# Optimization experiments

Hardware: AMD Instinct MI355X
Metric: run time of the kernel (lower is better)

Reference implementation:

```python
import jax, jax.numpy as jnp
import numpy as np

D = 1024   # hidden
H = 4      # heads
HD = D // H
E = 8      # experts
FF = 4096  # expert ffn dim
CAP_FACTOR = 1.0


def _ln(x, g, b, eps=1e-5):
    mu = jnp.mean(x, -1, keepdims=True)
    v = jnp.mean((x - mu) ** 2, -1, keepdims=True)
    return (x - mu) * jax.lax.rsqrt(v + eps) * g + b


def setup_inputs() -> dict:
    key = jax.random.key(0)
    ks = jax.random.split(key, 8)
    L, N = 1024, 16
    s = 0.02
    return {
        "x": jax.random.normal(ks[0], (L, N, D), jnp.float32),
        "in_proj_w": jax.random.normal(ks[1], (3 * D, D), jnp.float32) * s,
        "in_proj_b": jnp.zeros((3 * D,), jnp.float32),
        "out_proj_w": jax.random.normal(ks[2], (D, D), jnp.float32) * s,
        "out_proj_b": jnp.zeros((D,), jnp.float32),
        "ln1_g": jnp.ones((D,), jnp.float32),
        "ln1_b": jnp.zeros((D,), jnp.float32),
        "ln2_g": jnp.ones((D,), jnp.float32),
        "ln2_b": jnp.zeros((D,), jnp.float32),
        "wg": jax.random.normal(ks[3], (D, E), jnp.float32) * s,
        "w1": jax.random.normal(ks[4], (E, D, FF), jnp.float32) * s,
        "b1": jnp.zeros((E, FF), jnp.float32),
        "w2": jax.random.normal(ks[5], (E, FF, D), jnp.float32) * s,
        "b2": jnp.zeros((E, D), jnp.float32),
    }


def _mha(x, w, b, ow, ob):
    # x: [L, N, D] (torch MultiheadAttention layout, batch_first=False)
    L, N, _ = x.shape
    qkv = x @ w.T + b
    q, k, v = jnp.split(qkv, 3, axis=-1)
    rh = lambda t: t.reshape(L, N, H, HD).transpose(1, 2, 0, 3)  # -> [N,H,L,HD]
    q, k, v = rh(q), rh(k), rh(v)
    scores = jnp.einsum('nhld,nhmd->nhlm', q, k) / np.float32(np.sqrt(HD))
    attn = jax.nn.softmax(scores, axis=-1)
    o = jnp.einsum('nhlm,nhmd->nhld', attn, v).transpose(2, 0, 1, 3).reshape(L, N, D)
    return o @ ow.T + ob


def _moe(x, wg, w1, b1, w2, b2):
    # top-1 switch gating with capacity drop, dispatch, grouped GEMM, combine
    L, N, _ = x.shape
    S = L * N
    cap = int(CAP_FACTOR * S) // E  # 2048
    xf = x.reshape(S, D)
    gates = jax.nn.softmax(xf @ wg, axis=-1)           # [S,E]
    idx = jnp.argmax(gates, axis=-1)                    # [S] top-1 expert
    mask1 = jax.nn.one_hot(idx, E, dtype=x.dtype)       # [S,E]
    # position of each token within its expert's queue
    loc = jnp.sum((jnp.cumsum(mask1, 0) - 1.0) * mask1, -1).astype(jnp.int32)
    keep = loc < cap                                    # capacity drop mask
    gate_val = jnp.take_along_axis(gates, idx[:, None], -1)[:, 0]
    slot = jnp.where(keep, idx.astype(jnp.int32) * cap + loc, E * cap)  # OOB if dropped
    disp = jnp.zeros((E * cap, D), x.dtype).at[slot].set(xf, mode='drop')
    disp = disp.reshape(E, cap, D)
    # expert = Linear(D,FF) -> Linear(FF,D), NO activation between (per source)
    h = jnp.einsum('ecd,edf->ecf', disp, w1) + b1[:, None, :]
    y = (jnp.einsum('ecf,efd->ecd', h, w2) + b2[:, None, :]).reshape(E * cap, D)
    out = jnp.where(keep[:, None], gate_val[:, None] * y[jnp.minimum(slot, E * cap - 1)], 0.0)
    return out.reshape(L, N, D)


def reference(x, in_proj_w, in_proj_b, out_proj_w, out_proj_b,
              ln1_g, ln1_b, ln2_g, ln2_b, wg, w1, b1, w2, b2):
    y1 = _ln(x + _mha(x, in_proj_w, in_proj_b, out_proj_w, out_proj_b), ln1_g, ln1_b)
    y2 = _ln(y1 + _moe(y1, wg, w1, b1, w2, b2), ln2_g, ln2_b)
    return y2
```

## Files before the change

### kernel.cpp

```cpp
#include <hip/hip_runtime.h>
#include <hip/hip_bf16.h>

typedef __bf16 bf16_t;
typedef bf16_t bf16x4 __attribute__((ext_vector_type(4)));
typedef bf16_t bf16x8 __attribute__((ext_vector_type(8)));
typedef float  f32x4  __attribute__((ext_vector_type(4)));
typedef _Float16 half4 __attribute__((ext_vector_type(4)));
typedef _Float16 half8 __attribute__((ext_vector_type(8)));

#define L_  1024
#define N_  16
#define S_  16384
#define D_  1024
#define H_  4
#define HD_ 256
#define E_  8
#define FF_ 4096
#define CAP_ 2048
#define ESLOTS_ (E_*CAP_)
#define TAU_ 0.03f

__device__ __forceinline__ void gload16(const void* g, void* l) {
  __builtin_amdgcn_global_load_lds(
      (const __attribute__((address_space(1))) void*)g,
      (__attribute__((address_space(3))) void*)l,
      16, 0, 0);
}

#define SRC_SWZ(lane) (((lane) & 3) ^ (((lane) >> 3) & 3))

__global__ __launch_bounds__(256) void split2(
    const float* __restrict__ in, _Float16* __restrict__ oh,
    _Float16* __restrict__ ol, long n4)
{
  long i = (long)blockIdx.x * blockDim.x + threadIdx.x;
  long stride = (long)gridDim.x * blockDim.x;
  for (; i < n4; i += stride) {
    float4 v = ((const float4*)in)[i];
    half4 h, l;
    h.x = (_Float16)v.x; l.x = (_Float16)((v.x - (float)h.x) * 4096.0f);
    h.y = (_Float16)v.y; l.y = (_Float16)((v.y - (float)h.y) * 4096.0f);
    h.z = (_Float16)v.z; l.z = (_Float16)((v.z - (float)h.z) * 4096.0f);
    h.w = (_Float16)v.w; l.w = (_Float16)((v.w - (float)h.w) * 4096.0f);
    ((half4*)oh)[i] = h;
    ((half4*)ol)[i] = l;
  }
}

template<int EPI, bool HAS_BIAS, int PROD>
__global__ __launch_bounds__(256) void hgemm3s(
    const _Float16* __restrict__ Ah, const _Float16* __restrict__ Al,
    const _Float16* __restrict__ Bh, const _Float16* __restrict__ Bl,
    float* __restrict__ Cf, _Float16* __restrict__ Ch, _Float16* __restrict__ Cl,
    const float* __restrict__ bias,
    int K, long lda, long ldb, long ldcf, long ldch,
    int Z2, long sA1, long sA2, long sB1, long sB2, long sC1, long sC2, long sBias)
{
  constexpr int NL   = (PROD == 3) ? 2 : 1;
  constexpr int NBUF = (PROD == 3) ? 2 : 3;
  __shared__ _Float16 tA[NL][NBUF][128 * 32];
  __shared__ _Float16 tB[NL][NBUF][64 * 32];
  const int z  = blockIdx.z;
  const int z1 = z / Z2, z2 = z - z1 * Z2;
  const long aoff = (long)z1 * sA1 + (long)z2 * sA2;
  const long boff = (long)z1 * sB1 + (long)z2 * sB2;
  const long coff = (long)z1 * sC1 + (long)z2 * sC2;
  const int brow = blockIdx.y * 128, bcol = blockIdx.x * 64;
  const int tid = threadIdx.x, lane = tid & 63, wid = tid >> 6;
  const int wr = (wid >> 1) * 64, wc = (wid & 1) * 32;
  const int fr = lane & 15;
  const int fqs = (((lane >> 4) ^ ((fr >> 1) & 3)) * 8);

  const bool isA = (wid < 2);
  int limb, dstoff, nch;
  const _Float16* ssrc;
  if constexpr (PROD == 3) {
    limb = wid & 1; nch = isA ? 8 : 4; dstoff = 0;
    ssrc = (wid == 0) ? Ah : (wid == 1) ? Al : (wid == 2) ? Bh : Bl;
  } else {
    limb = 0; nch = isA ? 4 : 2; dstoff = (wid & 1) * nch;
    ssrc = isA ? Ah : Bh;
  }
  const long sld = isA ? lda : ldb;
  const long soff = isA ? aoff : boff;
  int srow = (isA ? brow : bcol) + (lane >> 2);
  if constexpr (PROD == 1) srow += (wid & 1) * (isA ? 64 : 32);
  const _Float16* sbase = ssrc + soff + (long)srow * sld + SRC_SWZ(lane) * 8;

  f32x4 acc0[4][2], acc1[4][2];
#pragma unroll
  for (int mi = 0; mi < 4; ++mi)
#pragma unroll
    for (int ni = 0; ni < 2; ++ni) {
      acc0[mi][ni] = f32x4{0.f, 0.f, 0.f, 0.f};
      acc1[mi][ni] = f32x4{0.f, 0.f, 0.f, 0.f};
    }

  const int NT = K >> 5;

  if constexpr (PROD == 3) {
    {
      _Float16* d0 = (isA ? &tA[limb][0][0] : &tB[limb][0][0]) + dstoff * 512;
      for (int i = 0; i < nch; ++i)
        gload16(sbase + (long)(16 * i) * sld, d0 + i * 512);
    }
    __syncthreads();

    for (int t = 0; t < NT; ++t) {
      const int cur = t & 1;
      if (t + 1 < NT) {
        const int k1 = (t + 1) * 32;
        _Float16* d0 = (isA ? &tA[limb][cur ^ 1][0] : &tB[limb][cur ^ 1][0]) + dstoff * 512;
        for (int i = 0; i < nch; ++i)
          gload16(sbase + (long)(16 * i) * sld + k1, d0 + i * 512);
      }

      half8 bh_[2], bl_[2];
#pragma unroll
      for (int ni = 0; ni < 2; ++ni) {
        bh_[ni] = *(const half8*)&tB[0][cur][(wc + ni * 16 + fr) * 32 + fqs];
        bl_[ni] = *(const half8*)&tB[1][cur][(wc + ni * 16 + fr) * 32 + fqs];
      }
      half8 ah_[4], al_[4];
#pragma unroll
      for (int mi = 0; mi < 4; ++mi) {
        ah_[mi] = *(const half8*)&tA[0][cur][(wr + mi * 16 + fr) * 32 + fqs];
        al_[mi] = *(const half8*)&tA[1][cur][(wr + mi * 16 + fr) * 32 + fqs];
      }
#pragma unroll
      for (int mi = 0; mi < 4; ++mi)
#pragma unroll
        for (int ni = 0; ni < 2; ++ni)
          acc0[mi][ni] = __builtin_amdgcn_mfma_f32_16x16x32_f16(ah_[mi], bh_[ni], acc0[mi][ni], 0, 0, 0);
#pragma unroll
      for (int mi = 0; mi < 4; ++mi)
#pragma unroll
        for (int ni = 0; ni < 2; ++ni)
          acc1[mi][ni] = __builtin_amdgcn_mfma_f32_16x16x32_f16(ah_[mi], bl_[ni], acc1[mi][ni], 0, 0, 0);
#pragma unroll
      for (int mi = 0; mi < 4; ++mi)
#pragma unroll
        for (int ni = 0; ni < 2; ++ni)
          acc1[mi][ni] = __builtin_amdgcn_mfma_f32_16x16x32_f16(al_[mi], bh_[ni], acc1[mi][ni], 0, 0, 0);
      __syncthreads();
    }
  } else {
    {
      _Float16* d0 = (isA ? &tA[0][0][0] : &tB[0][0][0]) + dstoff * 512;
      for (int i = 0; i < nch; ++i)
        gload16(sbase + (long)(16 * i) * sld, d0 + i * 512);
      _Float16* d1 = (isA ? &tA[0][1][0] : &tB[0][1][0]) + dstoff * 512;
      for (int i = 0; i < nch; ++i)
        gload16(sbase + (long)(16 * i) * sld + 32, d1 + i * 512);
    }
    if (isA) asm volatile("s_waitcnt vmcnt(4)" ::: "memory");
    else     asm volatile("s_waitcnt vmcnt(2)" ::: "memory");
    __builtin_amdgcn_s_barrier();

    for (int t = 0; t < NT; ++t) {
      const int b = t % 3;
      if (t + 2 < NT) {
        const int k2 = (t + 2) * 32;
        const int b2 = (t + 2) % 3;
        _Float16* d0 = (isA ? &tA[0][b2][0] : &tB[0][b2][0]) + dstoff * 512;
        for (int i = 0; i < nch; ++i)
          gload16(sbase + (long)(16 * i) * sld + k2, d0 + i * 512);
      }

      half8 bh_[2];
#pragma unroll
      for (int ni = 0; ni < 2; ++ni)
        bh_[ni] = *(const half8*)&tB[0][b][(wc + ni * 16 + fr) * 32 + fqs];
      half8 ah_[4];
#pragma unroll
      for (int mi = 0; mi < 4; ++mi)
        ah_[mi] = *(const half8*)&tA[0][b][(wr + mi * 16 + fr) * 32 + fqs];
#pragma unroll
      for (int mi = 0; mi < 4; ++mi)
#pragma unroll
        for (int ni = 0; ni < 2; ++ni)
          acc0[mi][ni] = __builtin_amdgcn_mfma_f32_16x16x32_f16(ah_[mi], bh_[ni], acc0[mi][ni], 0, 0, 0);

      if (t + 1 < NT) {
        if (t + 2 < NT) {
          if (isA) asm volatile("s_waitcnt vmcnt(4)" ::: "memory");
          else     asm volatile("s_waitcnt vmcnt(2)" ::: "memory");
        } else {
          asm volatile("s_waitcnt vmcnt(0)" ::: "memory");
        }
        __builtin_amdgcn_s_barrier();
      }
    }
  }

#pragma unroll
  for (int mi = 0; mi < 4; ++mi) {
#pragma unroll
    for (int ni = 0; ni < 2; ++ni) {
      int gcol = bcol + wc + ni * 16 + fr;
      float bv = 0.0f;
      if constexpr (HAS_BIAS) bv = bias[(long)z1 * sBias + gcol];
#pragma unroll
      for (int v = 0; v < 4; ++v) {
        int grow = brow + wr + mi * 16 + (lane >> 4) * 4 + v;
        float val = acc0[mi][ni][v] + bv;
        if constexpr (PROD == 3) val += acc1[mi][ni][v] * 0.000244140625f;
        if constexpr (EPI == 0) {
          Cf[coff + (long)grow * ldcf + gcol] = val;
        } else if constexpr (EPI == 1) {
          _Float16 hh = (_Float16)val;
          _Float16 ll = (_Float16)((val - (float)hh) * 4096.0f);
          long ci = coff + (long)grow * ldch + gcol;
          Ch[ci] = hh; Cl[ci] = ll;
        } else if constexpr (EPI == 3) {
          Ch[coff + (long)grow * ldch + gcol] = (_Float16)val;
        } else {
          if (bcol < 2048) {
            _Float16 hh = (_Float16)val;
            _Float16 ll = (_Float16)((val - (float)hh) * 4096.0f);
            long ci = (long)grow * ldch + gcol;
            Ch[ci] = hh; Cl[ci] = ll;
          } else {
            Cf[(long)grow * ldcf + (gcol - 2048)] = val;
          }
        }
      }
    }
  }
}

template<bool OUT_BF16, bool HAS_BIAS>
__global__ __launch_bounds__(256) void bgemm16(
    const bf16_t* __restrict__ A, const bf16_t* __restrict__ B,
    void* __restrict__ Cout, const float* __restrict__ bias,
    int K, long lda, long ldb, long ldc,
    long sA1, long sB1, long sC1, long sBias)
{
  __shared__ bf16_t tiles[2][3][128 * 32];
  const int z = blockIdx.z;
  const long coff = (long)z * sC1;
  const int brow = blockIdx.y * 128, bcol = blockIdx.x * 128;
  const int tid = threadIdx.x, lane = tid & 63, wid = tid >> 6;
  const int wr = (wid >> 1) * 64, wc = (wid & 1) * 64;
  const int fr = lane & 15;
  const int fqs = (((lane >> 4) ^ ((fr >> 1) & 3)) * 8);

  const bf16_t* src0 = (wid < 2) ? (A + (long)z * sA1) : (B + (long)z * sB1);
  const long ld = (wid < 2) ? lda : ldb;
  const int  rb = ((wid < 2) ? brow : bcol) + 64 * (wid & 1) + (lane >> 2);
  const bf16_t* srcbase = src0 + (long)rb * ld + SRC_SWZ(lane) * 8;
  const int tsel = wid >> 1, halfsel = wid & 1;

  f32x4 acc[4][4];
#pragma unroll
  for (int mi = 0; mi < 4; ++mi)
#pragma unroll
    for (int ni = 0; ni < 4; ++ni)
      acc[mi][ni] = f32x4{0.0f, 0.0f, 0.0f, 0.0f};

  const int NT = K >> 5;

#pragma unroll
  for (int i = 0; i < 4; ++i)
    gload16(srcbase + (long)(16 * i) * ld, &tiles[tsel][0][(4 * halfsel + i) * 512]);
#pragma unroll
  for (int i = 0; i < 4; ++i)
    gload16(srcbase + (long)(16 * i) * ld + 32, &tiles[tsel][1][(4 * halfsel + i) * 512]);
  asm volatile("s_waitcnt vmcnt(4)" ::: "memory");
  __builtin_amdgcn_s_barrier();

  for (int t = 0; t < NT; ++t) {
    const int b = t % 3;
    if (t + 2 < NT) {
      const int k2 = (t + 2) * 32;
      const int b2 = (t + 2) % 3;
#pragma unroll
      for (int i = 0; i < 4; ++i)
        gload16(srcbase + (long)(16 * i) * ld + k2, &tiles[tsel][b2][(4 * halfsel + i) * 512]);
    }

    bf16x8 af[4], bfv[4];
#pragma unroll
    for (int i = 0; i < 4; ++i) {
      af[i]  = *(const bf16x8*)&tiles[0][b][(wr + i * 16 + fr) * 32 + fqs];
      bfv[i] = *(const bf16x8*)&tiles[1][b][(wc + i * 16 + fr) * 32 + fqs];
    }
#pragma unroll
    for (int mi = 0; mi < 4; ++mi)
#pragma unroll
      for (int ni = 0; ni < 4; ++ni)
        acc[mi][ni] = __builtin_amdgcn_mfma_f32_16x16x32_bf16(af[mi], bfv[ni], acc[mi][ni], 0, 0, 0);

    if (t + 1 < NT) {
      if (t + 2 < NT) asm volatile("s_waitcnt vmcnt(4)" ::: "memory");
      else            asm volatile("s_waitcnt vmcnt(0)" ::: "memory");
      __builtin_amdgcn_s_barrier();
    }
  }

#pragma unroll
  for (int mi = 0; mi < 4; ++mi) {
#pragma unroll
    for (int ni = 0; ni < 4; ++ni) {
      int gcol = bcol + wc + ni * 16 + fr;
      float bv = 0.0f;
      if constexpr (HAS_BIAS) bv = bias[(long)z * sBias + gcol];
#pragma unroll
      for (int v = 0; v < 4; ++v) {
        int grow = brow + wr + mi * 16 + (lane >> 4) * 4 + v;
        float val = acc[mi][ni][v] + bv;
        long ci = coff + (long)grow * ldc + gcol;
        if constexpr (OUT_BF16) ((bf16_t*)Cout)[ci] = (bf16_t)val;
        else                    ((float*)Cout)[ci]  = val;
      }
    }
  }
}

template<typename TOUT>
__global__ __launch_bounds__(256) void transpose_f32(
    const float* __restrict__ src, TOUT* __restrict__ dst,
    long ld_src, long ld_dst, int Z2,
    long ss1, long ss2, long sd1, long sd2)
{
  __shared__ float t[32][33];
  const int z = blockIdx.z, z1 = z / Z2, z2 = z - z1 * Z2;
  src += (long)z1 * ss1 + (long)z2 * ss2;
  dst += (long)z1 * sd1 + (long)z2 * sd2;
  const int c0 = blockIdx.x * 32, r0 = blockIdx.y * 32;
  const int tx = threadIdx.x & 31, ty = threadIdx.x >> 5;
#pragma unroll
  for (int i = 0; i < 4; ++i)
    t[ty + i * 8][tx] = src[(long)(r0 + ty + i * 8) * ld_src + c0 + tx];
  __syncthreads();
#pragma unroll
  for (int i = 0; i < 4; ++i)
    dst[(long)(c0 + ty + i * 8) * ld_dst + r0 + tx] = (TOUT)t[tx][ty + i * 8];
}

__global__ __launch_bounds__(256) void transpose_split(
    const float* __restrict__ src, _Float16* __restrict__ dh, _Float16* __restrict__ dl,
    long ld_src, long ld_dst, int Z2,
    long ss1, long ss2, long sd1, long sd2)
{
  __shared__ float t[32][33];
  const int z = blockIdx.z, z1 = z / Z2, z2 = z - z1 * Z2;
  src += (long)z1 * ss1 + (long)z2 * ss2;
  dh  += (long)z1 * sd1 + (long)z2 * sd2;
  dl  += (long)z1 * sd1 + (long)z2 * sd2;
  const int c0 = blockIdx.x * 32, r0 = blockIdx.y * 32;
  const int tx = threadIdx.x & 31, ty = threadIdx.x >> 5;
#pragma unroll
  for (int i = 0; i < 4; ++i)
    t[ty + i * 8][tx] = src[(long)(r0 + ty + i * 8) * ld_src + c0 + tx];
  __syncthreads();
#pragma unroll
  for (int i = 0; i < 4; ++i) {
    float v = t[tx][ty + i * 8];
    _Float16 h = (_Float16)v;
    _Float16 l = (_Float16)((v - (float)h) * 4096.0f);
    long idx = (long)(c0 + ty + i * 8) * ld_dst + r0 + tx;
    dh[idx] = h;
    dl[idx] = l;
  }
}

__global__ __launch_bounds__(256) void softmax16(
    _Float16* __restrict__ Sm, float scale)
{
  __shared__ float red[4];
  const long row = blockIdx.x;
  half4* p = (half4*)(Sm + row * 1024);
  const int tid = threadIdx.x;
  half4 hv = p[tid];
  float v0 = (float)hv.x, v1 = (float)hv.y, v2 = (float)hv.z, v3 = (float)hv.w;
  float m = fmaxf(fmaxf(v0, v1), fmaxf(v2, v3));
#pragma unroll
  for (int o = 32; o; o >>= 1) m = fmaxf(m, __shfl_xor(m, o, 64));
  if ((tid & 63) == 0) red[tid >> 6] = m;
  __syncthreads();
  m = fmaxf(fmaxf(red[0], red[1]), fmaxf(red[2], red[3]));
  __syncthreads();
  float e0 = __expf((v0 - m) * scale);
  float e1 = __expf((v1 - m) * scale);
  float e2 = __expf((v2 - m) * scale);
  float e3 = __expf((v3 - m) * scale);
  float s = e0 + e1 + e2 + e3;
#pragma unroll
  for (int o = 32; o; o >>= 1) s += __shfl_xor(s, o, 64);
  if ((tid & 63) == 0) red[tid >> 6] = s;
  __syncthreads();
  s = red[0] + red[1] + red[2] + red[3];
  float inv = 1.0f / s;
  half4 w;
  w.x = (_Float16)(e0 * inv); w.y = (_Float16)(e1 * inv);
  w.z = (_Float16)(e2 * inv); w.w = (_Float16)(e3 * inv);
  p[tid] = w;
}

template<bool WRITE_LO>
__global__ __launch_bounds__(256) void softmax_pack(
    float* __restrict__ Sm, float scale)
{
  __shared__ float red[4];
  const long row = blockIdx.x;
  const float4* p = (const float4*)(Sm + row * 1024);
  const int tid = threadIdx.x;
  float4 v = p[tid];
  float m = fmaxf(fmaxf(v.x, v.y), fmaxf(v.z, v.w));
#pragma unroll
  for (int o = 32; o; o >>= 1) m = fmaxf(m, __shfl_xor(m, o, 64));
  if ((tid & 63) == 0) red[tid >> 6] = m;
  __syncthreads();
  m = fmaxf(fmaxf(red[0], red[1]), fmaxf(red[2], red[3]));
  __syncthreads();
  float e0 = __expf((v.x - m) * scale);
  float e1 = __expf((v.y - m) * scale);
  float e2 = __expf((v.z - m) * scale);
  float e3 = __expf((v.w - m) * scale);
  float s = e0 + e1 + e2 + e3;
#pragma unroll
  for (int o = 32; o; o >>= 1) s += __shfl_xor(s, o, 64);
  if ((tid & 63) == 0) red[tid >> 6] = s;
  __syncthreads();
  s = red[0] + red[1] + red[2] + red[3];
  float inv = 1.0f / s;
  float p0 = e0 * inv, p1 = e1 * inv, p2 = e2 * inv, p3 = e3 * inv;
  half4 h;
  h.x = (_Float16)p0; h.y = (_Float16)p1; h.z = (_Float16)p2; h.w = (_Float16)p3;
  _Float16* base = (_Float16*)Sm + row * 2048;
  ((half4*)base)[tid] = h;
  if constexpr (WRITE_LO) {
    half4 l;
    l.x = (_Float16)((p0 - (float)h.x) * 4096.0f);
    l.y = (_Float16)((p1 - (float)h.y) * 4096.0f);
    l.z = (_Float16)((p2 - (float)h.z) * 4096.0f);
    l.w = (_Float16)((p3 - (float)h.w) * 4096.0f);
    ((half4*)(base + 1024))[tid] = l;
  }
}

__global__ __launch_bounds__(256) void add_ln_gate(
    const float* __restrict__ x, const float* __restrict__ attn,
    const float* __restrict__ g, const float* __restrict__ be,
    const float* __restrict__ wg, bf16_t* __restrict__ yb,
    int* __restrict__ idx, float* __restrict__ gval,
    int* __restrict__ bcnt16, int* __restrict__ blist16)
{
  __shared__ float red[4];
  __shared__ float lred[4][8];
  const long s = blockIdx.x;
  const int tid = threadIdx.x;
  const int lane = tid & 63, w = tid >> 6;
  float4 va = ((const float4*)(x + s * 1024))[tid];
  float4 vb = ((const float4*)(attn + s * 1024))[tid];
  float v0 = va.x + vb.x, v1 = va.y + vb.y, v2 = va.z + vb.z, v3 = va.w + vb.w;
  float sum = v0 + v1 + v2 + v3;
#pragma unroll
  for (int o = 32; o; o >>= 1) sum += __shfl_xor(sum, o, 64);
  if (lane == 0) red[w] = sum;
  __syncthreads();
  float mu = (red[0] + red[1] + red[2] + red[3]) * (1.0f / 1024.0f);
  __syncthreads();
  float d0 = v0 - mu, d1 = v1 - mu, d2 = v2 - mu, d3 = v3 - mu;
  float ss = d0 * d0 + d1 * d1 + d2 * d2 + d3 * d3;
#pragma unroll
  for (int o = 32; o; o >>= 1) ss += __shfl_xor(ss, o, 64);
  if (lane == 0) red[w] = ss;
  __syncthreads();
  float var = (red[0] + red[1] + red[2] + red[3]) * (1.0f / 1024.0f);
  float rstd = rsqrtf(var + 1e-5f);
  float4 vg  = ((const float4*)g)[tid];
  float4 vbe = ((const float4*)be)[tid];
  float y0 = d0 * rstd * vg.x + vbe.x;
  float y1v = d1 * rstd * vg.y + vbe.y;
  float y2v = d2 * rstd * vg.z + vbe.z;
  float y3 = d3 * rstd * vg.w + vbe.w;
  bf16x4 ov = { (bf16_t)y0, (bf16_t)y1v, (bf16_t)y2v, (bf16_t)y3 };
  *(bf16x4*)(yb + s * 1024 + tid * 4) = ov;
  float lg[8];
  const float* w0 = wg + (long)(tid * 4) * 8;
#pragma unroll
  for (int e = 0; e < 8; ++e)
    lg[e] = y0 * w0[e] + y1v * w0[8 + e] + y2v * w0[16 + e] + y3 * w0[24 + e];
#pragma unroll
  for (int e = 0; e < 8; ++e) {
#pragma unroll
    for (int o = 32; o; o >>= 1) lg[e] += __shfl_xor(lg[e], o, 64);
  }
  if (lane == 0) {
#pragma unroll
    for (int e = 0; e < 8; ++e) lred[w][e] = lg[e];
  }
  __syncthreads();
  if (tid == 0) {
    float Lg[8];
#pragma unroll
    for (int e = 0; e < 8; ++e)
      Lg[e] = lred[0][e] + lred[1][e] + lred[2][e] + lred[3][e];
    float best = Lg[0], second = -1e30f; int bi = 0;
#pragma unroll
    for (int e = 1; e < 8; ++e) {
      if (Lg[e] > best) { second = best; best = Lg[e]; bi = e; }
      else if (Lg[e] > second) second = Lg[e];
    }
    float sm = 0.0f;
#pragma unroll
    for (int e = 0; e < 8; ++e) sm += __expf(Lg[e] - best);
    idx[s] = bi;
    gval[s] = 1.0f / sm;
    if (best - second < TAU_) {
      int n = (int)(s & 15);
      int p = atomicAdd(&bcnt16[n], 1);
      if (p < 128) blist16[n * 128 + p] = (int)s;
    }
  }
}

__global__ void zero16(int* __restrict__ p)
{
  if (threadIdx.x < 16) p[threadIdx.x] = 0;
}

__global__ __launch_bounds__(64) void qp_gather(
    const int* __restrict__ bcnt16, const int* __restrict__ blist16,
    const _Float16* __restrict__ QKh, const _Float16* __restrict__ QKl,
    _Float16* __restrict__ Qph, _Float16* __restrict__ Qpl)
{
  const int b = blockIdx.x;
  const int n = b >> 7, p = b & 127;
  const int t = threadIdx.x;
  half8* dh = (half8*)(Qph + (long)b * 1024);
  half8* dl = (half8*)(Qpl + (long)b * 1024);
  int cnt = bcnt16[n]; if (cnt > 128) cnt = 128;
  if (p < cnt) {
    long srow = (long)blist16[b] * 2048;
    const half8* sh = (const half8*)(QKh + srow);
    const half8* sl = (const half8*)(QKl + srow);
    dh[t * 2]     = sh[t * 2];
    dh[t * 2 + 1] = sh[t * 2 + 1];
    dl[t * 2]     = sl[t * 2];
    dl[t * 2 + 1] = sl[t * 2 + 1];
  } else {
    half8 z;
#pragma unroll
    for (int i = 0; i < 8; ++i) z[i] = (_Float16)0.0f;
    dh[t * 2] = z; dh[t * 2 + 1] = z;
    dl[t * 2] = z; dl[t * 2 + 1] = z;
  }
}

__global__ __launch_bounds__(256) void gate_fix(
    const int* __restrict__ bcnt16, const int* __restrict__ blist16,
    const float* __restrict__ attn_p, const float* __restrict__ x,
    const float* __restrict__ g, const float* __restrict__ be,
    const float* __restrict__ wg,
    int* __restrict__ idx, float* __restrict__ gval)
{
  const int b = blockIdx.x;
  const int n = b >> 7, p = b & 127;
  int cnt = bcnt16[n]; if (cnt > 128) cnt = 128;
  if (p >= cnt) return;
  const long s = blist16[b];
  __shared__ float red[4];
  __shared__ float lred[4][8];
  const int tid = threadIdx.x;
  const int lane = tid & 63, w = tid >> 6;
  float4 va = ((const float4*)(x + s * 1024))[tid];
  float4 vb = ((const float4*)(attn_p + (long)b * 1024))[tid];
  float v0 = va.x + vb.x, v1 = va.y + vb.y, v2 = va.z + vb.z, v3 = va.w + vb.w;
  float sum = v0 + v1 + v2 + v3;
#pragma unroll
  for (int o = 32; o; o >>= 1) sum += __shfl_xor(sum, o, 64);
  if (lane == 0) red[w] = sum;
  __syncthreads();
  float mu = (red[0] + red[1] + red[2] + red[3]) * (1.0f / 1024.0f);
  __syncthreads();
  float d0 = v0 - mu, d1 = v1 - mu, d2 = v2 - mu, d3 = v3 - mu;
  float ss = d0 * d0 + d1 * d1 + d2 * d2 + d3 * d3;
#pragma unroll
  for (int o = 32; o; o >>= 1) ss += __shfl_xor(ss, o, 64);
  if (lane == 0) red[w] = ss;
  __syncthreads();
  float var = (red[0] + red[1] + red[2] + red[3]) * (1.0f / 1024.0f);
  float rstd = rsqrtf(var + 1e-5f);
  float4 vg  = ((const float4*)g)[tid];
  float4 vbe = ((const float4*)be)[tid];
  float y0 = d0 * rstd * vg.x + vbe.x;
  float y1v = d1 * rstd * vg.y + vbe.y;
  float y2v = d2 * rstd * vg.z + vbe.z;
  float y3 = d3 * rstd * vg.w + vbe.w;
  float lg[8];
  const float* w0 = wg + (long)(tid * 4) * 8;
#pragma unroll
  for (int e = 0; e < 8; ++e)
    lg[e] = y0 * w0[e] + y1v * w0[8 + e] + y2v * w0[16 + e] + y3 * w0[24 + e];
#pragma unroll
  for (int e = 0; e < 8; ++e) {
#pragma unroll
    for (int o = 32; o; o >>= 1) lg[e] += __shfl_xor(lg[e], o, 64);
  }
  if (lane == 0) {
#pragma unroll
    for (int e = 0; e < 8; ++e) lred[w][e] = lg[e];
  }
  __syncthreads();
  if (tid == 0) {
    float Lg[8];
#pragma unroll
    for (int e = 0; e < 8; ++e)
      Lg[e] = lred[0][e] + lred[1][e] + lred[2][e] + lred[3][e];
    float best = Lg[0]; int bi = 0;
#pragma unroll
    for (int e = 1; e < 8; ++e) { if (Lg[e] > best) { best = Lg[e]; bi = e; } }
    float sm = 0.0f;
#pragma unroll
    for (int e = 0; e < 8; ++e) sm += __expf(Lg[e] - best);
    idx[s] = bi;
    gval[s] = 1.0f / sm;
  }
}

__global__ __launch_bounds__(256) void combine_ln(
    const bf16_t* __restrict__ y1b, const bf16_t* __restrict__ ymoe,
    const int* __restrict__ slot, const float* __restrict__ gval,
    const float* __restrict__ g, const float* __restrict__ be,
    float* __restrict__ out)
{
  __shared__ float red[4];
  const long s = blockIdx.x;
  const int tid = threadIdx.x;
  const int lane = tid & 63, w = tid >> 6;
  int sl = slot[s];
  bool keep = sl < ESLOTS_;
  float gv = keep ? gval[s] : 0.0f;
  long mrow = keep ? (long)sl * 1024 : 0;
  bf16x4 ya = *(const bf16x4*)(y1b + s * 1024 + tid * 4);
  bf16x4 ym = *(const bf16x4*)(ymoe + mrow + tid * 4);
  float v0 = (float)ya[0] + gv * (float)ym[0];
  float v1 = (float)ya[1] + gv * (float)ym[1];
  float v2 = (float)ya[2] + gv * (float)ym[2];
  float v3 = (float)ya[3] + gv * (float)ym[3];
  float sum = v0 + v1 + v2 + v3;
#pragma unroll
  for (int o = 32; o; o >>= 1) sum += __shfl_xor(sum, o, 64);
  if (lane == 0) red[w] = sum;
  __syncthreads();
  float mu = (red[0] + red[1] + red[2] + red[3]) * (1.0f / 1024.0f);
  __syncthreads();
  float d0 = v0 - mu, d1 = v1 - mu, d2 = v2 - mu, d3 = v3 - mu;
  float ss = d0 * d0 + d1 * d1 + d2 * d2 + d3 * d3;
#pragma unroll
  for (int o = 32; o; o >>= 1) ss += __shfl_xor(ss, o, 64);
  if (lane == 0) red[w] = ss;
  __syncthreads();
  float var = (red[0] + red[1] + red[2] + red[3]) * (1.0f / 1024.0f);
  float rstd = rsqrtf(var + 1e-5f);
  float4 vg  = ((const float4*)g)[tid];
  float4 vbe = ((const float4*)be)[tid];
  float4 ov = {d0 * rstd * vg.x + vbe.x, d1 * rstd * vg.y + vbe.y,
               d2 * rstd * vg.z + vbe.z, d3 * rstd * vg.w + vbe.w};
  ((float4*)(out + s * 1024))[tid] = ov;
}

__global__ __launch_bounds__(128) void rs_count(
    const int* __restrict__ idx, int* __restrict__ bcounts, int* __restrict__ tfs)
{
  __shared__ int cnt[8];
  const int b = blockIdx.x, t = threadIdx.x;
  if (t < 8) cnt[t] = 0;
  __syncthreads();
  int e = idx[b * 128 + t];
  atomicAdd(&cnt[e], 1);
  tfs[b * 128 + t] = -1;
  __syncthreads();
  if (t < 8) bcounts[b * 8 + t] = cnt[t];
}

__global__ __launch_bounds__(64) void rs_scan(
    const int* __restrict__ bcounts, int* __restrict__ boffs)
{
  const int e = threadIdx.x;
  if (e < 8) {
    int acc = 0;
    for (int b = 0; b < 128; ++b) {
      boffs[b * 8 + e] = acc;
      acc += bcounts[b * 8 + e];
    }
  }
}

__global__ __launch_bounds__(128) void rs_emit(
    const int* __restrict__ idx, const int* __restrict__ boffs,
    int* __restrict__ slot, int* __restrict__ tfs)
{
  __shared__ int le[128];
  const int b = blockIdx.x, t = threadIdx.x;
  const int s = b * 128 + t;
  int e = idx[s];
  le[t] = e;
  __syncthreads();
  int loc = boffs[b * 8 + e];
  for (int u = 0; u < t; ++u) loc += (le[u] == e) ? 1 : 0;
  int sl = (loc < CAP_) ? e * CAP_ + loc : ESLOTS_;
  slot[s] = sl;
  if (sl < ESLOTS_) tfs[sl] = s;
}

__global__ void dispatch_rows(
    const int* __restrict__ tfs, const bf16_t* __restrict__ y1b,
    bf16_t* __restrict__ disp)
{
  const int row = blockIdx.x;
  const int t = tfs[row];
  bf16x8* d = (bf16x8*)(disp + (long)row * 1024);
  if (t >= 0) {
    const bf16x8* sp = (const bf16x8*)(y1b + (long)t * 1024);
    d[threadIdx.x] = sp[threadIdx.x];
  } else {
    bf16x8 zv;
#pragma unroll
    for (int i = 0; i < 8; ++i) zv[i] = (bf16_t)0.0f;
    d[threadIdx.x] = zv;
  }
}

__global__ void fill_val(float* __restrict__ p, float v, long n)
{
  long i = (long)blockIdx.x * blockDim.x + threadIdx.x;
  long stride = (long)gridDim.x * blockDim.x;
  for (; i < n; i += stride) p[i] = v;
}

extern "C" void kernel_launch(void* const* d_in, const int* in_sizes, int n_in,
                              void* d_out, int out_size, void* d_ws, size_t ws_size,
                              hipStream_t stream)
{
  const float* x    = (const float*)d_in[0];
  const float* Wqkv = (const float*)d_in[1];
  const float* bqkv = (const float*)d_in[2];
  const float* Wo   = (const float*)d_in[3];
  const float* bo   = (const float*)d_in[4];
  const float* g1   = (const float*)d_in[5];
  const float* b1n  = (const float*)d_in[6];
  const float* g2   = (const float*)d_in[7];
  const float* b2n  = (const float*)d_in[8];
  const float* wg   = (const float*)d_in[9];
  const float* w1   = (const float*)d_in[10];
  const float* b1e  = (const float*)d_in[11];
  const float* w2   = (const float*)d_in[12];
  const float* b2e  = (const float*)d_in[13];
  float* out = (float*)d_out;

  const size_t MB = 1ull << 20;
  const size_t REQUIRED = 384 * MB;
  if (ws_size < REQUIRED) {
    fill_val<<<2048, 256, 0, stream>>>(out, (float)(ws_size >> 20), (long)out_size);
    return;
  }

  char* ws = (char*)d_ws;
  _Float16* Xh   = (_Float16*)(ws + 0);
  _Float16* Xl   = (_Float16*)(ws + 32 * MB);
  _Float16* Wqh  = (_Float16*)(ws + 64 * MB);
  _Float16* Wql  = (_Float16*)(ws + 70 * MB);
  _Float16* scores16 = (_Float16*)(ws + 0);
  _Float16* Woh  = (_Float16*)(ws + 64 * MB);
  _Float16* Wol  = (_Float16*)(ws + 66 * MB);
  _Float16* QKh  = (_Float16*)(ws + 80 * MB);
  _Float16* QKl  = (_Float16*)(ws + 144 * MB);
  float*    Vf32 = (float*)(ws + 208 * MB);
  _Float16* oh   = (_Float16*)(ws + 208 * MB);
  _Float16* vTh  = (_Float16*)(ws + 272 * MB);
  _Float16* vTl  = (_Float16*)(ws + 304 * MB);
  float*    attn = (float*)(ws + 0);
  bf16_t*   y1b  = (bf16_t*)(ws + 208 * MB);
  float*    scp   = (float*)(ws + 0);
  _Float16* Qph   = (_Float16*)(ws + 32 * MB);
  _Float16* Qpl   = (_Float16*)(ws + 36 * MB);
  _Float16* o_ph  = (_Float16*)(ws + 40 * MB);
  _Float16* o_pl  = (_Float16*)(ws + 44 * MB);
  float*    attnp = (float*)(ws + 48 * MB);
  int*      idx  = (int*)(ws + 336 * MB);
  int*      slot = idx + S_;
  float*    gval = (float*)(slot + S_);
  int*      tfs  = (int*)(gval + S_);
  int*      bcnt16  = tfs + S_;
  int*      blist16 = bcnt16 + 16;
  int*      bcounts = blist16 + 2048;
  int*      boffs   = bcounts + 1024;
  bf16_t*   disp = (bf16_t*)(ws + 272 * MB);
  bf16_t*   W1t  = (bf16_t*)(ws + 0);
  bf16_t*   W2t  = (bf16_t*)(ws + 0);
  bf16_t*   h    = (bf16_t*)(ws + 80 * MB);
  bf16_t*   ymoe = (bf16_t*)(ws + 304 * MB);

  zero16<<<1, 64, 0, stream>>>(bcnt16);

  split2<<<4096, 256, 0, stream>>>(x, Xh, Xl, (long)S_ * D_ / 4);
  split2<<<2048, 256, 0, stream>>>(Wqkv, Wqh, Wql, (long)3 * D_ * D_ / 4);

  hgemm3s<2, true, 3><<<dim3(48, 128, 1), 256, 0, stream>>>(
      Xh, Xl, Wqh, Wql, Vf32, QKh, QKl, bqkv,
      D_, D_, D_, D_, 2 * D_,
      1, 0, 0, 0, 0, 0, 0, 0);

  split2<<<1024, 256, 0, stream>>>(Wo, Woh, Wol, (long)D_ * D_ / 4);

  transpose_split<<<dim3(HD_ / 32, L_ / 32, 64), 256, 0, stream>>>(
      Vf32, vTh, vTl, (long)N_ * D_, L_,
      H_, D_, HD_, (long)H_ * HD_ * L_, (long)HD_ * L_);

  for (int g = 0; g < 2; ++g) {
    const long qko = (long)g * 8 * 2048;
    hgemm3s<3, false, 1><<<dim3(16, 8, 32), 256, 0, stream>>>(
        QKh + qko, QKl + qko, QKh + qko + 1024, QKl + qko + 1024,
        nullptr, scores16, nullptr, nullptr,
        HD_, (long)N_ * 2048, (long)N_ * 2048, 0, L_,
        H_, 2048, 256, 2048, 256, (long)H_ * L_ * L_, (long)L_ * L_, 0);
    softmax16<<<8 * H_ * L_, 256, 0, stream>>>(scores16, 0.0625f);
    hgemm3s<3, false, 1><<<dim3(4, 8, 32), 256, 0, stream>>>(
        scores16, nullptr,
        vTh + (long)g * 8 * H_ * HD_ * L_, vTl + (long)g * 8 * H_ * HD_ * L_,
        nullptr, oh + (long)g * 8 * D_, nullptr, nullptr,
        L_, L_, L_, 0, (long)N_ * D_,
        H_, (long)H_ * L_ * L_, (long)L_ * L_,
        (long)H_ * HD_ * L_, (long)HD_ * L_, D_, HD_, 0);
  }

  hgemm3s<0, true, 1><<<dim3(16, 128, 1), 256, 0, stream>>>(
      oh, nullptr, Woh, Wol, attn, nullptr, nullptr, bo,
      D_, D_, D_, D_, 0,
      1, 0, 0, 0, 0, 0, 0, 0);

  add_ln_gate<<<S_, 256, 0, stream>>>(x, attn, g1, b1n, wg, y1b,
                                      idx, gval, bcnt16, blist16);

  qp_gather<<<2048, 64, 0, stream>>>(bcnt16, blist16, QKh, QKl, Qph, Qpl);
  hgemm3s<0, false, 3><<<dim3(16, 1, 64), 256, 0, stream>>>(
      Qph, Qpl, QKh + 1024, QKl + 1024, scp, nullptr, nullptr, nullptr,
      HD_, 1024, (long)N_ * 2048, 1024, 0,
      4, (long)128 * 1024, 256, 2048, 256,
      (long)4 * 128 * 1024, (long)128 * 1024, 0);
  softmax_pack<true><<<64 * 128, 256, 0, stream>>>(scp, 0.0625f);
  hgemm3s<1, false, 3><<<dim3(4, 1, 64), 256, 0, stream>>>(
      (_Float16*)scp, (_Float16*)scp + 1024, vTh, vTl,
      nullptr, o_ph, o_pl, nullptr,
      L_, 2048, L_, 0, 1024,
      4, (long)4 * 128 * 2048, (long)128 * 2048,
      (long)H_ * HD_ * L_, (long)HD_ * L_,
      (long)128 * 1024, 256, 0);
  hgemm3s<0, true, 3><<<dim3(16, 16, 1), 256, 0, stream>>>(
      o_ph, o_pl, Woh, Wol, attnp, nullptr, nullptr, bo,
      D_, D_, D_, D_, 0,
      1, 0, 0, 0, 0, 0, 0, 0);
  gate_fix<<<2048, 256, 0, stream>>>(bcnt16, blist16, attnp, x,
                                     g1, b1n, wg, idx, gval);

  rs_count<<<128, 128, 0, stream>>>(idx, bcounts, tfs);
  rs_scan<<<1, 64, 0, stream>>>(bcounts, boffs);
  rs_emit<<<128, 128, 0, stream>>>(idx, boffs, slot, tfs);

  dispatch_rows<<<ESLOTS_, 128, 0, stream>>>(tfs, y1b, disp);

  transpose_f32<bf16_t><<<dim3(FF_ / 32, D_ / 32, E_), 256, 0, stream>>>(
      w1, W1t, FF_, D_, 1, (long)D_ * FF_, 0, (long)FF_ * D_, 0);

  bgemm16<true, true><<<dim3(32, 16, 8), 256, 0, stream>>>(
      disp, W1t, h, b1e, D_, D_, D_, FF_,
      (long)CAP_ * D_, (long)FF_ * D_, (long)CAP_ * FF_, FF_);

  transpose_f32<bf16_t><<<dim3(D_ / 32, FF_ / 32, E_), 256, 0, stream>>>(
      w2, W2t, D_, FF_, 1, (long)FF_ * D_, 0, (long)D_ * FF_, 0);

  bgemm16<true, true><<<dim3(8, 16, 8), 256, 0, stream>>>(
      h, W2t, ymoe, b2e, FF_, FF_, FF_, D_,
      (long)CAP_ * FF_, (long)D_ * FF_, (long)CAP_ * D_, D_);

  combine_ln<<<S_, 256, 0, stream>>>(y1b, ymoe, slot, gval, g2, b2n, out);
}
```

Before: 1.477 ms.

## Fuse token dispatch gather into expert GEMM via indirect A-row loads

Removes the dispatch_rows kernel that copied routed token rows into a dense expert buffer. The first expert GEMM now reads A rows straight from y1b through the token-for-slot table, and empty slots point at a small zeroed row. This saves writing and rereading a 32 MB dispatch buffer and one launch. It also adds s_setprio around the MFMA block to favor the compute waves. The cost is a per-thread table lookup and four base pointers held in registers.

```diff
diff --git a/kernel.cpp b/kernel.cpp
--- a/kernel.cpp
+++ b/kernel.cpp
@@ -229,12 +229,13 @@
   }
 }
 
-template<bool OUT_BF16, bool HAS_BIAS>
+template<bool OUT_BF16, bool HAS_BIAS, bool IND_A>
 __global__ __launch_bounds__(256) void bgemm16(
     const bf16_t* __restrict__ A, const bf16_t* __restrict__ B,
     void* __restrict__ Cout, const float* __restrict__ bias,
     int K, long lda, long ldb, long ldc,
-    long sA1, long sB1, long sC1, long sBias)
+    long sA1, long sB1, long sC1, long sBias,
+    const int* __restrict__ tfs, const bf16_t* __restrict__ zrow)
 {
   __shared__ bf16_t tiles[2][3][128 * 32];
   const int z = blockIdx.z;
@@ -245,11 +246,24 @@
   const int fr = lane & 15;
   const int fqs = (((lane >> 4) ^ ((fr >> 1) & 3)) * 8);
 
-  const bf16_t* src0 = (wid < 2) ? (A + (long)z * sA1) : (B + (long)z * sB1);
-  const long ld = (wid < 2) ? lda : ldb;
-  const int  rb = ((wid < 2) ? brow : bcol) + 64 * (wid & 1) + (lane >> 2);
-  const bf16_t* srcbase = src0 + (long)rb * ld + SRC_SWZ(lane) * 8;
   const int tsel = wid >> 1, halfsel = wid & 1;
+
+  const bf16_t* cbase[4];
+#pragma unroll
+  for (int i = 0; i < 4; ++i) {
+    if (tsel == 0) {
+      int row_i = brow + 64 * halfsel + 16 * i + (lane >> 2);
+      if constexpr (IND_A) {
+        int tok = tfs[z * CAP_ + row_i];
+        cbase[i] = ((tok >= 0) ? (A + (long)tok * 1024) : zrow) + SRC_SWZ(lane) * 8;
+      } else {
+        cbase[i] = A + (long)z * sA1 + (long)row_i * lda + SRC_SWZ(lane) * 8;
+      }
+    } else {
+      int row_i = bcol + 64 * halfsel + 16 * i + (lane >> 2);
+      cbase[i] = B + (long)z * sB1 + (long)row_i * ldb + SRC_SWZ(lane) * 8;
+    }
+  }
 
   f32x4 acc[4][4];
 #pragma unroll
@@ -262,10 +276,10 @@
 
 #pragma unroll
   for (int i = 0; i < 4; ++i)
-    gload16(srcbase + (long)(16 * i) * ld, &tiles[tsel][0][(4 * halfsel + i) * 512]);
+    gload16(cbase[i], &tiles[tsel][0][(4 * halfsel + i) * 512]);
 #pragma unroll
   for (int i = 0; i < 4; ++i)
-    gload16(srcbase + (long)(16 * i) * ld + 32, &tiles[tsel][1][(4 * halfsel + i) * 512]);
+    gload16(cbase[i] + 32, &tiles[tsel][1][(4 * halfsel + i) * 512]);
   asm volatile("s_waitcnt vmcnt(4)" ::: "memory");
   __builtin_amdgcn_s_barrier();
 
@@ -276,7 +290,7 @@
       const int b2 = (t + 2) % 3;
 #pragma unroll
       for (int i = 0; i < 4; ++i)
-        gload16(srcbase + (long)(16 * i) * ld + k2, &tiles[tsel][b2][(4 * halfsel + i) * 512]);
+        gload16(cbase[i] + k2, &tiles[tsel][b2][(4 * halfsel + i) * 512]);
     }
 
     bf16x8 af[4], bfv[4];
@@ -285,11 +299,13 @@
       af[i]  = *(const bf16x8*)&tiles[0][b][(wr + i * 16 + fr) * 32 + fqs];
       bfv[i] = *(const bf16x8*)&tiles[1][b][(wc + i * 16 + fr) * 32 + fqs];
     }
+    __builtin_amdgcn_s_setprio(1);
 #pragma unroll
     for (int mi = 0; mi < 4; ++mi)
 #pragma unroll
       for (int ni = 0; ni < 4; ++ni)
         acc[mi][ni] = __builtin_amdgcn_mfma_f32_16x16x32_bf16(af[mi], bfv[ni], acc[mi][ni], 0, 0, 0);
+    __builtin_amdgcn_s_setprio(0);
 
     if (t + 1 < NT) {
       if (t + 2 < NT) asm volatile("s_waitcnt vmcnt(4)" ::: "memory");
@@ -705,24 +721,6 @@
   int sl = (loc < CAP_) ? e * CAP_ + loc : ESLOTS_;
   slot[s] = sl;
   if (sl < ESLOTS_) tfs[sl] = s;
-}
-
-__global__ void dispatch_rows(
-    const int* __restrict__ tfs, const bf16_t* __restrict__ y1b,
-    bf16_t* __restrict__ disp)
-{
-  const int row = blockIdx.x;
-  const int t = tfs[row];
-  bf16x8* d = (bf16x8*)(disp + (long)row * 1024);
-  if (t >= 0) {
-    const bf16x8* sp = (const bf16x8*)(y1b + (long)t * 1024);
-    d[threadIdx.x] = sp[threadIdx.x];
-  } else {
-    bf16x8 zv;
-#pragma unroll
-    for (int i = 0; i < 8; ++i) zv[i] = (bf16_t)0.0f;
-    d[threadIdx.x] = zv;
-  }
 }
 
 __global__ void fill_val(float* __restrict__ p, float v, long n)
@@ -789,13 +787,14 @@
   int*      blist16 = bcnt16 + 16;
   int*      bcounts = blist16 + 2048;
   int*      boffs   = bcounts + 1024;
-  bf16_t*   disp = (bf16_t*)(ws + 272 * MB);
+  bf16_t*   zrow = (bf16_t*)(ws + 337 * MB);
   bf16_t*   W1t  = (bf16_t*)(ws + 0);
   bf16_t*   W2t  = (bf16_t*)(ws + 0);
   bf16_t*   h    = (bf16_t*)(ws + 80 * MB);
   bf16_t*   ymoe = (bf16_t*)(ws + 304 * MB);
 
   zero16<<<1, 64, 0, stream>>>(bcnt16);
+  fill_val<<<1, 256, 0, stream>>>((float*)zrow, 0.0f, 512);
 
   split2<<<4096, 256, 0, stream>>>(x, Xh, Xl, (long)S_ * D_ / 4);
   split2<<<2048, 256, 0, stream>>>(Wqkv, Wqh, Wql, (long)3 * D_ * D_ / 4);
@@ -861,21 +860,19 @@
   rs_scan<<<1, 64, 0, stream>>>(bcounts, boffs);
   rs_emit<<<128, 128, 0, stream>>>(idx, boffs, slot, tfs);
 
-  dispatch_rows<<<ESLOTS_, 128, 0, stream>>>(tfs, y1b, disp);
-
   transpose_f32<bf16_t><<<dim3(FF_ / 32, D_ / 32, E_), 256, 0, stream>>>(
       w1, W1t, FF_, D_, 1, (long)D_ * FF_, 0, (long)FF_ * D_, 0);
 
-  bgemm16<true, true><<<dim3(32, 16, 8), 256, 0, stream>>>(
-      disp, W1t, h, b1e, D_, D_, D_, FF_,
-      (long)CAP_ * D_, (long)FF_ * D_, (long)CAP_ * FF_, FF_);
+  bgemm16<true, true, true><<<dim3(32, 16, 8), 256, 0, stream>>>(
+      y1b, W1t, h, b1e, D_, D_, D_, FF_,
+      0, (long)FF_ * D_, (long)CAP_ * FF_, FF_, tfs, zrow);
 
   transpose_f32<bf16_t><<<dim3(D_ / 32, FF_ / 32, E_), 256, 0, stream>>>(
       w2, W2t, D_, FF_, 1, (long)FF_ * D_, 0, (long)D_ * FF_, 0);
 
-  bgemm16<true, true><<<dim3(8, 16, 8), 256, 0, stream>>>(
+  bgemm16<true, true, false><<<dim3(8, 16, 8), 256, 0, stream>>>(
       h, W2t, ymoe, b2e, FF_, FF_, FF_, D_,
-      (long)CAP_ * FF_, (long)D_ * FF_, (long)CAP_ * D_, D_);
+      (long)CAP_ * FF_, (long)D_ * FF_, (long)CAP_ * D_, D_, nullptr, nullptr);
 
   combine_ln<<<S_, 256, 0, stream>>>(y1b, ymoe, slot, gval, g2, b2n, out);
 }
```

Result: no change. 1.477 ms (-0.0%).
